# Performance work log

Measured on AMD Instinct MI355X. Metric: run time of the kernel, lower is better.

The kernel has to match this reference:

```python
import jax, jax.numpy as jnp
import numpy as np
from jax import lax

# Constants matching PostProcess(conf_thres=0.4, iou_thres=0.5, merge=False, agnostic=False)
CONF_THRES = 0.4
IOU_THRES = 0.5
MAX_WH = 4096.0   # per-class box offset (agnostic=False)
MAX_DET = 300     # hardcoded in module
MAX_NMS = 30000   # cap on NMS candidates (yolov5 convention); JAX needs static shapes
B, N, NC = 16, 25200, 80


def setup_inputs() -> dict:
    key = jax.random.key(0)
    u = jax.random.uniform(key, (B, N, 5 + NC), dtype=jnp.float32)
    # cx,cy in [0,640); w,h in [2,102); obj and class scores in [0,1)
    scale = jnp.concatenate([jnp.array([640.0, 640.0, 100.0, 100.0], jnp.float32),
                             jnp.ones((1 + NC,), jnp.float32)])
    shift = jnp.concatenate([jnp.array([0.0, 0.0, 2.0, 2.0], jnp.float32),
                             jnp.zeros((1 + NC,), jnp.float32)])
    prediction = u * scale + shift
    return {"prediction": prediction}


def _cxcywh_to_xyxy(x):
    cx, cy, w, h = x[..., 0], x[..., 1], x[..., 2], x[..., 3]
    return jnp.stack([cx - 0.5 * w, cy - 0.5 * h, cx + 0.5 * w, cy + 0.5 * h], axis=-1)


def _process_one(x):  # x: [N, 5+NC]
    obj = x[:, 4]
    cls_conf = x[:, 5:] * obj[:, None]          # x[:,5:] *= x[:,4:5]
    box = _cxcywh_to_xyxy(x[:, :4])             # [N, 4]
    # multi-label candidate mask: obj > conf AND class conf > conf (x[xc] then x[:,5:] > conf)
    cand = (obj[:, None] > CONF_THRES) & (cls_conf > CONF_THRES)   # [N, NC]
    flat = jnp.where(cand, cls_conf, 0.0).reshape(-1)              # [N*NC]
    top_scores, top_idx = lax.top_k(flat, MAX_NMS)                 # static-size candidate set
    bi = top_idx // NC                                             # box index i
    cj = (top_idx % NC).astype(jnp.float32)                        # class index j
    cand_boxes = box[bi]                                           # [M, 4]
    scores0 = jnp.where(top_scores > CONF_THRES, top_scores, 0.0)  # 0 marks invalid/suppressed
    off_boxes = cand_boxes + cj[:, None] * MAX_WH                  # per-class offset for NMS
    areas = (off_boxes[:, 2] - off_boxes[:, 0]) * (off_boxes[:, 3] - off_boxes[:, 1])
    idx_range = jnp.arange(MAX_NMS)

    def step(scores, _):
        # greedy NMS: pick best remaining, suppress IoU > thresh (torchvision semantics)
        idx = jnp.argmax(scores)
        s = scores[idx]
        keep = s > 0.0
        b = off_boxes[idx]
        lt = jnp.maximum(b[:2], off_boxes[:, :2])
        rb = jnp.minimum(b[2:], off_boxes[:, 2:])
        wh = jnp.clip(rb - lt, 0.0)
        inter = wh[:, 0] * wh[:, 1]
        iou = inter / (areas[idx] + areas - inter + 1e-9)
        suppress = (iou > IOU_THRES) | (idx_range == idx)
        return jnp.where(suppress, 0.0, scores), (idx, keep)

    _, (keep_idx, keep_flag) = lax.scan(step, scores0, None, length=MAX_DET)
    rows = jnp.concatenate([cand_boxes[keep_idx],
                            top_scores[keep_idx][:, None],
                            cj[keep_idx][:, None]], axis=1)        # [MAX_DET, 6] = xyxy, conf, cls
    return jnp.where(keep_flag[:, None], rows, 0.0)


def reference(prediction):
    # Padded fixed-shape analogue of torch.stack(output): [B, MAX_DET, 6], zero rows = no detection
    return jax.vmap(_process_one)(prediction)
```

## Files before the change

kernel.cpp:

```cpp
#include <hip/hip_runtime.h>
#include <stdint.h>

#define BATCH 16
#define NROW 25200
#define NCLS 80
#define ROWF 85
#define MAXDET 300
#define MAXNMS 30000u
#define NBIN 3072
#define BASEBITS 0x3EC00000u
#define CAP 32768u
#define BATCH_FLOATS 2142000

#define PREBIN 2048
#define NBUCK 1024
#define CANDCAP 131072u
#define KMAX 2048u
#define TOPK 2048u
#define K2CAP 4096u

#define SORTCAP 1024
#define CH_SZ 128

#define TILE_ROWS 80
#define TILE_FLOATS 6800
#define RPB 400
#define SUBT 5
#define SBLK 63

#define ROWS_PER_BLK 256
#define SBLK2 99

__device__ __forceinline__ bool iou_gt_half(float ax1, float ay1, float ax2, float ay2, float aa,
                                            float bx1, float by1, float bx2, float by2, float ba) {
    float ltx = fmaxf(ax1, bx1), lty = fmaxf(ay1, by1);
    float rbx = fminf(ax2, bx2), rby = fminf(ay2, by2);
    float wx = fmaxf(__fsub_rn(rbx, ltx), 0.0f);
    float wy = fmaxf(__fsub_rn(rby, lty), 0.0f);
    float inter = __fmul_rn(wx, wy);
    float den = __fadd_rn(__fsub_rn(__fadd_rn(aa, ba), inter), 1e-9f);
    float t = __fmul_rn(0.5f, den);
    if (!(inter > t)) return false;
    float tg = __fmul_rn(0.50000012f, den);
    if (inter >= tg) return true;
    return __fdiv_rn(inter, den) > 0.5f;
}

__device__ __forceinline__ unsigned bin_of_bits(unsigned bits) {
    unsigned v = (bits - BASEBITS) >> 12;
    if (v > (unsigned)(NBIN - 1)) v = NBIN - 1;
    return v;
}

__global__ __launch_bounds__(256) void k_stage(const float* __restrict__ pred,
                                               unsigned* __restrict__ hist2,
                                               unsigned* __restrict__ ccnt,
                                               unsigned long long* __restrict__ cand,
                                               unsigned* __restrict__ oflow,
                                               int staged) {
    if (!staged) return;
    __shared__ unsigned shist[NBUCK];
    __shared__ unsigned long long skey[KMAX];
    __shared__ unsigned s_cnt, s_n, s_base;
    int bx = blockIdx.x;
    int b = bx / SBLK2, blk = bx - b * SBLK2;
    int t = threadIdx.x, lane = t & 63, wv = t >> 6;
    for (int i = t; i < NBUCK; i += 256) shist[i] = 0u;
    if (t == 0) s_cnt = 0u;
    __syncthreads();
    const float* pb = pred + (size_t)b * BATCH_FLOATS;
    int r0 = blk * ROWS_PER_BLK + wv * 64;
    int rown = NROW - r0;
    if (rown > 0) {
        if (rown > 64) rown = 64;
        float obj = 0.0f;
        if (lane < rown) obj = pb[(size_t)(r0 + lane) * ROWF + 4];
        unsigned long long live = __ballot(obj > 0.4f);
        while (live) {
            int j = (int)__builtin_ctzll(live);
            live &= live - 1ULL;
            float o = __shfl(obj, j);
            const float* rp = pb + (size_t)(r0 + j) * ROWF;
            unsigned grow = (unsigned)(r0 + j);
            {
                float s = __fmul_rn(rp[5 + lane], o);
                if (s >= 0.75f) {
                    unsigned bits = __float_as_uint(s);
                    unsigned bin = bin_of_bits(bits);
                    atomicAdd(&shist[bin - PREBIN], 1u);
                    unsigned u = atomicAdd(&s_cnt, 1u);
                    unsigned flat = grow * (unsigned)NCLS + (unsigned)lane;
                    if (u < KMAX)
                        skey[u] = ((unsigned long long)bits << 32) |
                                  (unsigned long long)(0xFFFFFFFFu - flat);
                    else oflow[b] = 1u;
                }
            }
            if (lane < 16) {
                int c = 64 + lane;
                float s = __fmul_rn(rp[5 + c], o);
                if (s >= 0.75f) {
                    unsigned bits = __float_as_uint(s);
                    unsigned bin = bin_of_bits(bits);
                    atomicAdd(&shist[bin - PREBIN], 1u);
                    unsigned u = atomicAdd(&s_cnt, 1u);
                    unsigned flat = grow * (unsigned)NCLS + (unsigned)c;
                    if (u < KMAX)
                        skey[u] = ((unsigned long long)bits << 32) |
                                  (unsigned long long)(0xFFFFFFFFu - flat);
                    else oflow[b] = 1u;
                }
            }
        }
    }
    __syncthreads();
    unsigned* gh = hist2 + (size_t)b * NBUCK;
    for (int i = t; i < NBUCK; i += 256) {
        unsigned v = shist[i];
        if (v) atomicAdd(&gh[i], v);
    }
    if (t == 0) {
        unsigned n = s_cnt;
        if (n > KMAX) n = KMAX;
        unsigned base = atomicAdd(&ccnt[b], n);
        if (base + n > CANDCAP) oflow[b] = 1u;
        s_n = n; s_base = base;
    }
    __syncthreads();
    unsigned n = s_n, base = s_base;
    if (base + n <= CANDCAP) {
        unsigned long long* cd = cand + (size_t)b * CANDCAP + base;
        for (unsigned k = t; k < n; k += 256) cd[k] = skey[k];
    }
}

__global__ __launch_bounds__(1024) void k_prep(const unsigned* __restrict__ hist2,
                                               const unsigned* __restrict__ ccnt,
                                               const unsigned* __restrict__ oflow,
                                               const unsigned long long* __restrict__ cand,
                                               unsigned* __restrict__ suf2,
                                               unsigned long long* __restrict__ keys2,
                                               int* __restrict__ meta,
                                               int staged) {
    __shared__ unsigned sS[NBUCK];
    __shared__ unsigned scur[NBUCK];
    __shared__ int s_cut, s_need, s_tot, s_T, s_valid;
    __shared__ unsigned s_bad, s_E;
    int b = blockIdx.x, t = threadIdx.x;
    unsigned h = hist2[(size_t)b * NBUCK + t];
    sS[t] = h;
    if (t == 0) { s_cut = -1; s_T = -1; s_bad = 0u; s_need = 0; s_tot = 0; s_E = 0u; }
    __syncthreads();
    if (h > (unsigned)SORTCAP) atomicOr(&s_bad, 1u);
    for (int off = 1; off < NBUCK; off <<= 1) {
        unsigned v = (t + off < NBUCK) ? sS[t + off] : 0u;
        __syncthreads();
        sS[t] += v;
        __syncthreads();
    }
    unsigned Sv = sS[t];
    unsigned Sn = (t + 1 < NBUCK) ? sS[t + 1] : 0u;
    if (Sv >= MAXNMS && Sn < MAXNMS) {
        s_cut = PREBIN + t; s_need = (int)(MAXNMS - Sn); s_tot = (int)Sv;
    }
    if (Sv >= TOPK && Sn < TOPK) { s_T = PREBIN + t; s_E = Sv; }
    unsigned* g2 = suf2 + (size_t)b * (NBUCK + 1);
    g2[t] = Sv;
    if (t == 0) g2[NBUCK] = 0u;
    scur[t] = Sn;
    __syncthreads();
    if (t == 0) {
        int valid = (staged && s_cut >= 0 && s_T >= 0 && s_bad == 0u &&
                     oflow[b] == 0u && ccnt[b] <= CANDCAP) ? 1 : 0;
        s_valid = valid;
        meta[b * 8 + 0] = valid ? s_cut : 0;
        meta[b * 8 + 1] = valid ? s_need : 0;
        meta[b * 8 + 2] = valid ? s_tot : 0;
        meta[b * 8 + 3] = valid;
        meta[b * 8 + 4] = valid ? s_T : 0;
        meta[b * 8 + 5] = valid ? (int)s_E : 0;
    }
    __syncthreads();
    if (s_valid) {
        int T = s_T;
        unsigned ccb = ccnt[b];
        const unsigned long long* cd = cand + (size_t)b * CANDCAP;
        unsigned long long* k2 = keys2 + (size_t)b * K2CAP;
        for (unsigned k = t; k < ccb; k += 1024) {
            unsigned long long key = cd[k];
            unsigned v = bin_of_bits((unsigned)(key >> 32));
            if ((int)v >= T) {
                unsigned pos = atomicAdd(&scur[v - PREBIN], 1u);
                if (pos < K2CAP) k2[pos] = key;
            }
        }
    }
}

__global__ __launch_bounds__(256) void k_hist_fb(const float* __restrict__ pred,
                                                 unsigned* __restrict__ hist,
                                                 const int* __restrict__ meta) {
    int bx = blockIdx.x;
    int b = bx / SBLK, blk = bx - b * SBLK;
    if (meta[b * 8 + 3]) return;
    __shared__ __align__(16) float rows[TILE_FLOATS];
    __shared__ unsigned shist[NBIN];
    int t = threadIdx.x, lane = t & 63, wv = t >> 6;
    for (int i = t; i < NBIN; i += 256) shist[i] = 0u;
    const float* pbase = pred + (size_t)b * BATCH_FLOATS + (size_t)blk * RPB * ROWF;
    for (int st = 0; st < SUBT; ++st) {
        __syncthreads();
        const float4* src = (const float4*)(pbase + (size_t)st * TILE_ROWS * ROWF);
        float4* dst = (float4*)rows;
        for (int i = t; i < TILE_FLOATS / 4; i += 256) dst[i] = src[i];
        __syncthreads();
        for (int r = wv; r < TILE_ROWS; r += 4) {
            float obj = rows[r * ROWF + 4];
            if (!(obj > 0.4f)) continue;
            for (int half = 0; half < 2; ++half) {
                int c = lane + (half << 6);
                if (c < NCLS) {
                    float s = __fmul_rn(rows[r * ROWF + 5 + c], obj);
                    if (s > 0.4f) atomicAdd(&shist[bin_of_bits(__float_as_uint(s))], 1u);
                }
            }
        }
    }
    __syncthreads();
    unsigned* gh = hist + (size_t)b * NBIN;
    for (int i = t; i < NBIN; i += 256) {
        unsigned v = shist[i];
        if (v) atomicAdd(&gh[i], v);
    }
}

__global__ __launch_bounds__(256) void k_scan_fb(const unsigned* __restrict__ hist,
                                                 unsigned* __restrict__ suf,
                                                 int* __restrict__ meta) {
    int b = blockIdx.x, t = threadIdx.x;
    if (meta[b * 8 + 3]) return;
    __shared__ unsigned sh[NBIN];
    __shared__ unsigned sS[NBIN];
    __shared__ unsigned cs[256];
    __shared__ int s_cut, s_need, s_tot;
    const unsigned* gh = hist + (size_t)b * NBIN;
    for (int i = t; i < NBIN; i += 256) sh[i] = gh[i];
    if (t == 0) { s_cut = 0; s_need = 0x7FFFFFFF; s_tot = 0; }
    __syncthreads();
    const int CHUNK = NBIN / 256;
    int base = t * CHUNK;
    unsigned tot = 0;
    for (int i = 0; i < CHUNK; ++i) tot += sh[base + i];
    cs[t] = tot;
    __syncthreads();
    for (int off = 1; off < 256; off <<= 1) {
        unsigned v = (t + off < 256) ? cs[t + off] : 0u;
        __syncthreads();
        cs[t] += v;
        __syncthreads();
    }
    unsigned after = (t + 1 < 256) ? cs[t + 1] : 0u;
    for (int i = CHUNK - 1; i >= 0; --i) {
        after += sh[base + i];
        sS[base + i] = after;
    }
    __syncthreads();
    unsigned* gs = suf + (size_t)b * (NBIN + 1);
    for (int i = t; i < NBIN; i += 256) gs[i] = sS[i];
    if (t == 0) gs[NBIN] = 0u;
    for (int i = 0; i < CHUNK; ++i) {
        int v = base + i;
        unsigned Sv = sS[v];
        unsigned Sn = (v + 1 < NBIN) ? sS[v + 1] : 0u;
        if (Sv >= MAXNMS && Sn < MAXNMS) {
            s_cut = v; s_need = (int)(MAXNMS - Sn); s_tot = (int)Sv;
        }
    }
    __syncthreads();
    if (t == 0) {
        int cut = s_cut, needv = s_need, totv = s_tot;
        if (sS[0] < MAXNMS) { cut = 0; needv = 0x7FFFFFFF; totv = (int)sS[0]; }
        meta[b * 8 + 0] = cut;
        meta[b * 8 + 1] = needv;
        meta[b * 8 + 2] = totv;
    }
}

__global__ __launch_bounds__(256) void k_scatter_fb(const float* __restrict__ pred,
                                                    const unsigned* __restrict__ suf,
                                                    const int* __restrict__ meta,
                                                    unsigned* __restrict__ cursor,
                                                    unsigned long long* __restrict__ keys) {
    int bx = blockIdx.x;
    int b = bx / SBLK, blk = bx - b * SBLK;
    if (meta[b * 8 + 3]) return;
    __shared__ __align__(16) float rows[TILE_FLOATS];
    int t = threadIdx.x, lane = t & 63, wv = t >> 6;
    int cutbin = meta[b * 8 + 0];
    const float* pbase = pred + (size_t)b * BATCH_FLOATS + (size_t)blk * RPB * ROWF;
    unsigned rowbase0 = (unsigned)(blk * RPB);
    const unsigned* gs = suf + (size_t)b * (NBIN + 1);
    unsigned* cur = cursor + (size_t)b * NBIN;
    unsigned long long* kb = keys + (size_t)b * CAP;
    for (int st = 0; st < SUBT; ++st) {
        __syncthreads();
        const float4* src = (const float4*)(pbase + (size_t)st * TILE_ROWS * ROWF);
        float4* dst = (float4*)rows;
        for (int i = t; i < TILE_FLOATS / 4; i += 256) dst[i] = src[i];
        __syncthreads();
        for (int r = wv; r < TILE_ROWS; r += 4) {
            float obj = rows[r * ROWF + 4];
            if (!(obj > 0.4f)) continue;
            unsigned grow = rowbase0 + (unsigned)(st * TILE_ROWS + r);
            for (int half = 0; half < 2; ++half) {
                int c = lane + (half << 6);
                if (c < NCLS) {
                    float s = __fmul_rn(rows[r * ROWF + 5 + c], obj);
                    if (s > 0.4f) {
                        unsigned bits = __float_as_uint(s);
                        unsigned bin = bin_of_bits(bits);
                        if ((int)bin >= cutbin) {
                            unsigned pos = gs[bin + 1] + atomicAdd(&cur[bin], 1u);
                            if (pos < CAP) {
                                unsigned flat = grow * (unsigned)NCLS + (unsigned)c;
                                kb[pos] = ((unsigned long long)bits << 32) |
                                          (unsigned long long)(0xFFFFFFFFu - flat);
                            }
                        }
                    }
                }
            }
        }
    }
}

__global__ __launch_bounds__(1024) void k_nms(const float* __restrict__ pred,
                                              const unsigned* __restrict__ suf,
                                              const unsigned* __restrict__ suf2,
                                              const int* __restrict__ meta,
                                              const unsigned* __restrict__ ccnt,
                                              const unsigned long long* __restrict__ keys,
                                              const unsigned long long* __restrict__ keys2,
                                              const unsigned long long* __restrict__ cand,
                                              float* __restrict__ out) {
    __shared__ unsigned sgsL[NBUCK + 1];
    __shared__ unsigned long long ktmp[SORTCAP];
    __shared__ unsigned long long skeys[SORTCAP];
    __shared__ unsigned maskW[CH_SZ][5];
    __shared__ unsigned sup0w[4];
    __shared__ float cbox[CH_SZ][9];
    __shared__ float kept[MAXDET][5];
    __shared__ int klist[MAXDET];
    __shared__ int s_nk, s_localk;
    __shared__ unsigned s_gc;

    int b = blockIdx.x;
    int tid = threadIdx.x;
    int lane = tid & 63, wv = tid >> 6;

    int cutbin = meta[b * 8 + 0];
    int needv  = meta[b * 8 + 1];
    unsigned total = (unsigned)meta[b * 8 + 2];
    int valid  = meta[b * 8 + 3];
    int Tbin   = meta[b * 8 + 4];
    unsigned E = valid ? (unsigned)meta[b * 8 + 5] : 0u;
    if (!valid && total > CAP) total = CAP;
    const unsigned* gs = suf + (size_t)b * (NBIN + 1);
    const unsigned* g2 = suf2 + (size_t)b * (NBUCK + 1);
    const unsigned long long* kb = keys + (size_t)b * CAP;
    const unsigned long long* k2 = keys2 + (size_t)b * K2CAP;
    const unsigned long long* cd = cand + (size_t)b * CANDCAP;
    unsigned ccb = valid ? ccnt[b] : 0u;
    if (ccb > CANDCAP) ccb = CANDCAP;
    const float* pb = pred + (size_t)b * BATCH_FLOATS;
    float* ob = out + (size_t)b * MAXDET * 6;

    if (valid) for (int i = tid; i < NBUCK + 1; i += 1024) sgsL[i] = g2[i];
    if (tid == 0) s_nk = 0;
    __syncthreads();

#define GSV(v) (valid ? sgsL[(v) - PREBIN] : gs[(v)])

    unsigned limit;
    if (needv == 0x7FFFFFFF) limit = total;
    else limit = GSV(cutbin + 1) + (unsigned)needv;
    if (limit > total) limit = total;

    unsigned p = 0;
    while (p < limit) {
        if (s_nk >= MAXDET) break;

        int lo = cutbin, hi = NBIN - 1, vs = NBIN - 1;
        while (lo <= hi) { int mid = (lo + hi) >> 1;
            if (GSV(mid) <= p + (unsigned)SORTCAP) { vs = mid; hi = mid - 1; } else lo = mid + 1; }
        unsigned gEnd = GSV(vs);
        bool phaseA = (!valid) || (p < E);
        if (valid && phaseA && gEnd > E) gEnd = E;
        if (gEnd > total) gEnd = total;
        if (gEnd <= p) { gEnd = p + (unsigned)SORTCAP; if (gEnd > total) gEnd = total; }
        unsigned G = gEnd - p;

        if (phaseA) {
            const unsigned long long* src = valid ? k2 : kb;
            unsigned myLo = 0, myHi = 0;
            unsigned long long raw = 0ULL;
            if (tid < (int)G) {
                unsigned idx = p + (unsigned)tid;
                int l2 = cutbin, h2 = NBIN - 1, v = cutbin;
                while (l2 <= h2) { int mid = (l2 + h2) >> 1;
                    if (GSV(mid) > idx) { v = mid; l2 = mid + 1; } else h2 = mid - 1; }
                unsigned bstart = GSV(v + 1);
                unsigned bend = GSV(v);
                raw = src[idx];
                myLo = (bstart > p) ? (bstart - p) : 0u;
                myHi = bend - p; if (myHi > G) myHi = G;
                ktmp[tid] = raw;
            }
            __syncthreads();
            if (tid < (int)G) {
                unsigned rank = 0;
                for (unsigned u = myLo; u < myHi; ++u) rank += (ktmp[u] > raw) ? 1u : 0u;
                skeys[myLo + rank] = raw;
            }
            __syncthreads();
        } else {
            int l0 = cutbin, h0 = NBIN - 1, w1 = cutbin;
            while (l0 <= h0) { int mid = (l0 + h0) >> 1;
                if (GSV(mid) > p) { w1 = mid; l0 = mid + 1; } else h0 = mid - 1; }
            if (tid == 0) s_gc = 0u;
            __syncthreads();
            for (unsigned k = tid; k < ccb; k += 1024) {
                unsigned long long key = cd[k];
                unsigned v = bin_of_bits((unsigned)(key >> 32));
                if ((int)v >= vs && (int)v <= w1) {
                    unsigned u = atomicAdd(&s_gc, 1u);
                    if (u < (unsigned)SORTCAP) ktmp[u] = key;
                }
            }
            __syncthreads();
            unsigned Gc = s_gc; if (Gc > (unsigned)SORTCAP) Gc = (unsigned)SORTCAP;
            if (tid < (int)Gc) {
                unsigned long long key = ktmp[tid];
                unsigned v = bin_of_bits((unsigned)(key >> 32));
                unsigned bstart = GSV(v + 1);
                unsigned rank = 0;
                for (unsigned u = 0; u < Gc; ++u) {
                    unsigned long long kk = ktmp[u];
                    unsigned vu = bin_of_bits((unsigned)(kk >> 32));
                    rank += (vu == v && kk > key) ? 1u : 0u;
                }
                skeys[(bstart - p) + rank] = key;
            }
            __syncthreads();
        }

        unsigned consumable = limit - p; if (consumable > G) consumable = G;

        for (unsigned c0 = 0; c0 < consumable; c0 += CH_SZ) {
            int nk0 = s_nk;
            if (nk0 >= MAXDET) break;
            int CH = (int)((consumable - c0 < (unsigned)CH_SZ) ? (consumable - c0) : (unsigned)CH_SZ);

            if (tid < CH_SZ * 5) maskW[tid / 5][tid % 5] = 0u;
            if (tid >= CH_SZ * 5 && tid < CH_SZ * 5 + 4) sup0w[tid - CH_SZ * 5] = 0u;
            if (tid < CH) {
                unsigned long long kk = skeys[c0 + tid];
                unsigned flat = 0xFFFFFFFFu - (unsigned)kk;
                unsigned bi = flat / (unsigned)NCLS;
                unsigned cc = flat - bi * (unsigned)NCLS;
                const float* rp = pb + (size_t)bi * ROWF;
                float cx = rp[0], cy = rp[1], wd = rp[2], ht = rp[3];
                float hw = __fmul_rn(0.5f, wd), hh = __fmul_rn(0.5f, ht);
                float off = __fmul_rn((float)cc, 4096.0f);
                float x1 = __fsub_rn(cx, hw), y1 = __fsub_rn(cy, hh);
                float x2 = __fadd_rn(cx, hw), y2 = __fadd_rn(cy, hh);
                float ox1 = __fadd_rn(x1, off), oy1 = __fadd_rn(y1, off);
                float ox2 = __fadd_rn(x2, off), oy2 = __fadd_rn(y2, off);
                cbox[tid][0] = ox1; cbox[tid][1] = oy1;
                cbox[tid][2] = ox2; cbox[tid][3] = oy2;
                cbox[tid][4] = __fmul_rn(__fsub_rn(ox2, ox1), __fsub_rn(oy2, oy1));
            }
            __syncthreads();

            {
                int col = tid & (CH_SZ - 1);
                int part = tid >> 7;
                if (col < CH) {
                    float bx1 = cbox[col][0], by1 = cbox[col][1];
                    float bx2 = cbox[col][2], by2 = cbox[col][3], ba = cbox[col][4];
                    unsigned part16 = 0u;
                    int rbase = part << 4;
                    for (int k = 0; k < 16; ++k) {
                        int i2 = rbase + k;
                        if (i2 >= col || i2 >= CH) break;
                        if (iou_gt_half(cbox[i2][0], cbox[i2][1], cbox[i2][2], cbox[i2][3],
                                        cbox[i2][4], bx1, by1, bx2, by2, ba))
                            part16 |= (1u << k);
                    }
                    if (part16)
                        atomicOr(&maskW[col][part >> 1], part16 << ((part & 1) << 4));
                    bool f = false;
                    for (int k2 = part; k2 < nk0; k2 += 8) {
                        if (iou_gt_half(kept[k2][0], kept[k2][1], kept[k2][2], kept[k2][3],
                                        kept[k2][4], bx1, by1, bx2, by2, ba)) f = true;
                    }
                    if (f) atomicOr(&sup0w[col >> 5], 1u << (col & 31));
                }
            }
            __syncthreads();

            if (wv == 0) {
                unsigned keptw = 0u;
                int nkv = nk0, lk = 0;
                unsigned pre0 = (lane < 4 && CH > 0) ? maskW[0][lane] : 0u;
                unsigned pre1 = (lane < 4 && CH > 1) ? maskW[1][lane] : 0u;
                for (int j = 0; j < CH && nkv < MAXDET; ++j) {
                    unsigned colw = pre0;
                    pre0 = pre1;
                    pre1 = (lane < 4 && (j + 2) < CH) ? maskW[j + 2][lane] : 0u;
                    bool hit = (keptw & colw) != 0u;
                    bool sup = __any(hit);
                    if ((sup0w[j >> 5] >> (j & 31)) & 1u) sup = true;
                    if (!sup) {
                        if (lane == (j >> 5)) keptw |= 1u << (j & 31);
                        if (lane == 0) klist[lk] = j;
                        lk++; nkv++;
                    }
                }
                if (lane == 0) { s_localk = lk; s_nk = nkv; }
            }
            __syncthreads();

            int lk = s_localk;
            for (int t2 = tid; t2 < lk; t2 += 1024) {
                int i = klist[t2];
                int oidx = nk0 + t2;
                kept[oidx][0] = cbox[i][0]; kept[oidx][1] = cbox[i][1];
                kept[oidx][2] = cbox[i][2]; kept[oidx][3] = cbox[i][3];
                kept[oidx][4] = cbox[i][4];
                unsigned long long kk = skeys[c0 + i];
                unsigned bits = (unsigned)(kk >> 32);
                unsigned flat = 0xFFFFFFFFu - (unsigned)kk;
                unsigned bi = flat / (unsigned)NCLS;
                unsigned cc = flat - bi * (unsigned)NCLS;
                const float* rp = pb + (size_t)bi * ROWF;
                float cx = rp[0], cy = rp[1], wd = rp[2], ht = rp[3];
                float hw = __fmul_rn(0.5f, wd), hh = __fmul_rn(0.5f, ht);
                float* orow = ob + (size_t)oidx * 6;
                orow[0] = __fsub_rn(cx, hw);
                orow[1] = __fsub_rn(cy, hh);
                orow[2] = __fadd_rn(cx, hw);
                orow[3] = __fadd_rn(cy, hh);
                orow[4] = __uint_as_float(bits);
                orow[5] = (float)cc;
            }
            __syncthreads();
        }
        p = gEnd;
    }
#undef GSV
}

extern "C" void kernel_launch(void* const* d_in, const int* in_sizes, int n_in,
                              void* d_out, int out_size, void* d_ws, size_t ws_size,
                              hipStream_t stream) {
    const float* pred = (const float*)d_in[0];
    float* outp = (float*)d_out;
    char* ws = (char*)d_ws;

    const size_t OFF_HIST  = 0;
    const size_t SZ_HIST   = (size_t)BATCH * NBIN * 4;
    const size_t OFF_CUR   = OFF_HIST + SZ_HIST;
    const size_t SZ_CUR    = (size_t)BATCH * NBIN * 4;
    const size_t OFF_H2    = OFF_CUR + SZ_CUR;
    const size_t SZ_H2     = (size_t)BATCH * NBUCK * 4;
    const size_t OFF_CCNT  = OFF_H2 + SZ_H2;
    const size_t SZ_CCNT   = (size_t)BATCH * 4;
    const size_t OFF_OFLW  = OFF_CCNT + SZ_CCNT;
    const size_t SZ_OFLW   = (size_t)BATCH * 4;
    const size_t OFF_META  = OFF_OFLW + SZ_OFLW;
    const size_t SZ_META   = (size_t)BATCH * 8 * 4;
    const size_t ZERO_SZ   = OFF_META + SZ_META;
    const size_t OFF_SUF   = ZERO_SZ;
    const size_t SZ_SUF    = (size_t)BATCH * (NBIN + 1) * 4;
    const size_t OFF_SUF2  = OFF_SUF + SZ_SUF;
    const size_t SZ_SUF2   = (size_t)BATCH * (NBUCK + 1) * 4;
    const size_t OFF_KEYS  = OFF_SUF2 + SZ_SUF2;
    const size_t SZ_KEYS   = (size_t)BATCH * CAP * 8;
    const size_t OFF_K2    = OFF_KEYS + SZ_KEYS;
    const size_t SZ_K2     = (size_t)BATCH * K2CAP * 8;
    const size_t OFF_CAND  = OFF_K2 + SZ_K2;
    const size_t SZ_CAND   = (size_t)BATCH * CANDCAP * 8;
    const size_t WS_NEEDED = OFF_CAND + SZ_CAND;

    int staged = (ws_size >= WS_NEEDED) ? 1 : 0;

    unsigned* hist             = (unsigned*)(ws + OFF_HIST);
    unsigned* cursor           = (unsigned*)(ws + OFF_CUR);
    unsigned* hist2            = (unsigned*)(ws + OFF_H2);
    unsigned* ccnt             = (unsigned*)(ws + OFF_CCNT);
    unsigned* oflow            = (unsigned*)(ws + OFF_OFLW);
    int* meta                  = (int*)(ws + OFF_META);
    unsigned* suf              = (unsigned*)(ws + OFF_SUF);
    unsigned* suf2             = (unsigned*)(ws + OFF_SUF2);
    unsigned long long* keys   = (unsigned long long*)(ws + OFF_KEYS);
    unsigned long long* keys2  = (unsigned long long*)(ws + OFF_K2);
    unsigned long long* cand   = (unsigned long long*)(ws + OFF_CAND);

    hipMemsetAsync(ws, 0, ZERO_SZ, stream);
    hipMemsetAsync(d_out, 0, (size_t)out_size * sizeof(float), stream);

    k_stage<<<dim3(BATCH * SBLK2), dim3(256), 0, stream>>>(pred, hist2, ccnt, cand, oflow, staged);
    k_prep<<<dim3(BATCH), dim3(1024), 0, stream>>>(hist2, ccnt, oflow, cand, suf2, keys2, meta, staged);
    k_hist_fb<<<dim3(BATCH * SBLK), dim3(256), 0, stream>>>(pred, hist, meta);
    k_scan_fb<<<dim3(BATCH), dim3(256), 0, stream>>>(hist, suf, meta);
    k_scatter_fb<<<dim3(BATCH * SBLK), dim3(256), 0, stream>>>(pred, suf, meta, cursor, keys);
    k_nms<<<dim3(BATCH), dim3(1024), 0, stream>>>(pred, suf, suf2, meta, ccnt, keys, keys2, cand, outp);
}
```

Baseline: 347.7 us.

## Flatten stage scan over elements and split candidate scatter into parallel kernel

The staging kernel now walks flat (row, class) elements across 128 blocks per batch, dropping the per-row obj ballot and early-skip, so every class element is read. The candidate scatter that used to run at the end of the single-block-per-batch prep kernel moves to a new kernel with 16 blocks per batch that uses global-memory atomics on bucket cursors. The aim is more parallelism in both phases. In exchange it loses the skip of rows with low objectness, reads the obj value once per element, adds global atomics and one more launch.

Result: no change. 349.8 us (+0.6%).

```diff
diff --git a/kernel.cpp b/kernel.cpp
--- a/kernel.cpp
+++ b/kernel.cpp
@@ -11,6 +11,7 @@
 #define BASEBITS 0x3EC00000u
 #define CAP 32768u
 #define BATCH_FLOATS 2142000
+#define NELEM 2016000u
 
 #define PREBIN 2048
 #define NBUCK 1024
@@ -22,14 +23,14 @@
 #define SORTCAP 1024
 #define CH_SZ 128
 
+#define SBLK3 128
+#define EPB (NELEM / SBLK3)
+
 #define TILE_ROWS 80
 #define TILE_FLOATS 6800
 #define RPB 400
 #define SUBT 5
 #define SBLK 63
-
-#define ROWS_PER_BLK 256
-#define SBLK2 99
 
 __device__ __forceinline__ bool iou_gt_half(float ax1, float ay1, float ax2, float ay2, float aa,
                                             float bx1, float by1, float bx2, float by2, float ba) {
@@ -63,54 +64,30 @@
     __shared__ unsigned long long skey[KMAX];
     __shared__ unsigned s_cnt, s_n, s_base;
     int bx = blockIdx.x;
-    int b = bx / SBLK2, blk = bx - b * SBLK2;
-    int t = threadIdx.x, lane = t & 63, wv = t >> 6;
+    int b = bx >> 7, blk = bx & (SBLK3 - 1);
+    int t = threadIdx.x;
     for (int i = t; i < NBUCK; i += 256) shist[i] = 0u;
     if (t == 0) s_cnt = 0u;
     __syncthreads();
     const float* pb = pred + (size_t)b * BATCH_FLOATS;
-    int r0 = blk * ROWS_PER_BLK + wv * 64;
-    int rown = NROW - r0;
-    if (rown > 0) {
-        if (rown > 64) rown = 64;
-        float obj = 0.0f;
-        if (lane < rown) obj = pb[(size_t)(r0 + lane) * ROWF + 4];
-        unsigned long long live = __ballot(obj > 0.4f);
-        while (live) {
-            int j = (int)__builtin_ctzll(live);
-            live &= live - 1ULL;
-            float o = __shfl(obj, j);
-            const float* rp = pb + (size_t)(r0 + j) * ROWF;
-            unsigned grow = (unsigned)(r0 + j);
-            {
-                float s = __fmul_rn(rp[5 + lane], o);
-                if (s >= 0.75f) {
-                    unsigned bits = __float_as_uint(s);
-                    unsigned bin = bin_of_bits(bits);
-                    atomicAdd(&shist[bin - PREBIN], 1u);
-                    unsigned u = atomicAdd(&s_cnt, 1u);
-                    unsigned flat = grow * (unsigned)NCLS + (unsigned)lane;
-                    if (u < KMAX)
-                        skey[u] = ((unsigned long long)bits << 32) |
-                                  (unsigned long long)(0xFFFFFFFFu - flat);
-                    else oflow[b] = 1u;
-                }
-            }
-            if (lane < 16) {
-                int c = 64 + lane;
-                float s = __fmul_rn(rp[5 + c], o);
-                if (s >= 0.75f) {
-                    unsigned bits = __float_as_uint(s);
-                    unsigned bin = bin_of_bits(bits);
-                    atomicAdd(&shist[bin - PREBIN], 1u);
-                    unsigned u = atomicAdd(&s_cnt, 1u);
-                    unsigned flat = grow * (unsigned)NCLS + (unsigned)c;
-                    if (u < KMAX)
-                        skey[u] = ((unsigned long long)bits << 32) |
-                                  (unsigned long long)(0xFFFFFFFFu - flat);
-                    else oflow[b] = 1u;
-                }
-            }
+    unsigned e0 = (unsigned)blk * EPB, e1 = e0 + EPB;
+    for (unsigned e = e0 + (unsigned)t; e < e1; e += 256u) {
+        unsigned row = e / (unsigned)NCLS;
+        unsigned c = e - row * (unsigned)NCLS;
+        unsigned rb = row * (unsigned)ROWF;
+        float obj = pb[rb + 4u];
+        float cv  = pb[rb + 5u + c];
+        float s = __fmul_rn(cv, obj);
+        if (s >= 0.75f) {
+            unsigned bits = __float_as_uint(s);
+            unsigned bin = bin_of_bits(bits);
+            atomicAdd(&shist[bin - PREBIN], 1u);
+            unsigned u = atomicAdd(&s_cnt, 1u);
+            unsigned flat = e;
+            if (u < KMAX)
+                skey[u] = ((unsigned long long)bits << 32) |
+                          (unsigned long long)(0xFFFFFFFFu - flat);
+            else oflow[b] = 1u;
         }
     }
     __syncthreads();
@@ -137,14 +114,12 @@
 __global__ __launch_bounds__(1024) void k_prep(const unsigned* __restrict__ hist2,
                                                const unsigned* __restrict__ ccnt,
                                                const unsigned* __restrict__ oflow,
-                                               const unsigned long long* __restrict__ cand,
                                                unsigned* __restrict__ suf2,
-                                               unsigned long long* __restrict__ keys2,
+                                               unsigned* __restrict__ gcur,
                                                int* __restrict__ meta,
                                                int staged) {
     __shared__ unsigned sS[NBUCK];
-    __shared__ unsigned scur[NBUCK];
-    __shared__ int s_cut, s_need, s_tot, s_T, s_valid;
+    __shared__ int s_cut, s_need, s_tot, s_T;
     __shared__ unsigned s_bad, s_E;
     int b = blockIdx.x, t = threadIdx.x;
     unsigned h = hist2[(size_t)b * NBUCK + t];
@@ -167,12 +142,11 @@
     unsigned* g2 = suf2 + (size_t)b * (NBUCK + 1);
     g2[t] = Sv;
     if (t == 0) g2[NBUCK] = 0u;
-    scur[t] = Sn;
+    gcur[(size_t)b * NBUCK + t] = Sn;
     __syncthreads();
     if (t == 0) {
         int valid = (staged && s_cut >= 0 && s_T >= 0 && s_bad == 0u &&
                      oflow[b] == 0u && ccnt[b] <= CANDCAP) ? 1 : 0;
-        s_valid = valid;
         meta[b * 8 + 0] = valid ? s_cut : 0;
         meta[b * 8 + 1] = valid ? s_need : 0;
         meta[b * 8 + 2] = valid ? s_tot : 0;
@@ -180,19 +154,31 @@
         meta[b * 8 + 4] = valid ? s_T : 0;
         meta[b * 8 + 5] = valid ? (int)s_E : 0;
     }
-    __syncthreads();
-    if (s_valid) {
-        int T = s_T;
-        unsigned ccb = ccnt[b];
-        const unsigned long long* cd = cand + (size_t)b * CANDCAP;
-        unsigned long long* k2 = keys2 + (size_t)b * K2CAP;
-        for (unsigned k = t; k < ccb; k += 1024) {
-            unsigned long long key = cd[k];
-            unsigned v = bin_of_bits((unsigned)(key >> 32));
-            if ((int)v >= T) {
-                unsigned pos = atomicAdd(&scur[v - PREBIN], 1u);
-                if (pos < K2CAP) k2[pos] = key;
-            }
+}
+
+__global__ __launch_bounds__(256) void k_scat2(const unsigned long long* __restrict__ cand,
+                                               const unsigned* __restrict__ ccnt,
+                                               const int* __restrict__ meta,
+                                               unsigned* __restrict__ gcur,
+                                               unsigned long long* __restrict__ keys2) {
+    int bx = blockIdx.x;
+    int b = bx >> 4, blk = bx & 15;
+    if (!meta[b * 8 + 3]) return;
+    int T = meta[b * 8 + 4];
+    unsigned ccb = ccnt[b];
+    if (ccb > CANDCAP) ccb = CANDCAP;
+    unsigned per = (ccb + 15u) >> 4;
+    unsigned s0 = (unsigned)blk * per, s1 = s0 + per;
+    if (s1 > ccb) s1 = ccb;
+    const unsigned long long* cd = cand + (size_t)b * CANDCAP;
+    unsigned long long* k2 = keys2 + (size_t)b * K2CAP;
+    unsigned* gc = gcur + (size_t)b * NBUCK;
+    for (unsigned k = s0 + threadIdx.x; k < s1; k += 256) {
+        unsigned long long key = cd[k];
+        unsigned v = bin_of_bits((unsigned)(key >> 32));
+        if ((int)v >= T) {
+            unsigned pos = atomicAdd(&gc[v - PREBIN], 1u);
+            if (pos < K2CAP) k2[pos] = key;
         }
     }
 }
@@ -362,7 +348,6 @@
     int needv  = meta[b * 8 + 1];
     unsigned total = (unsigned)meta[b * 8 + 2];
     int valid  = meta[b * 8 + 3];
-    int Tbin   = meta[b * 8 + 4];
     unsigned E = valid ? (unsigned)meta[b * 8 + 5] : 0u;
     if (!valid && total > CAP) total = CAP;
     const unsigned* gs = suf + (size_t)b * (NBIN + 1);
@@ -500,9 +485,9 @@
                     if (part16)
                         atomicOr(&maskW[col][part >> 1], part16 << ((part & 1) << 4));
                     bool f = false;
-                    for (int k2 = part; k2 < nk0; k2 += 8) {
-                        if (iou_gt_half(kept[k2][0], kept[k2][1], kept[k2][2], kept[k2][3],
-                                        kept[k2][4], bx1, by1, bx2, by2, ba)) f = true;
+                    for (int k2i = part; k2i < nk0; k2i += 8) {
+                        if (iou_gt_half(kept[k2i][0], kept[k2i][1], kept[k2i][2], kept[k2i][3],
+                                        kept[k2i][4], bx1, by1, bx2, by2, ba)) f = true;
                     }
                     if (f) atomicOr(&sup0w[col >> 5], 1u << (col & 31));
                 }
@@ -585,7 +570,9 @@
     const size_t SZ_SUF    = (size_t)BATCH * (NBIN + 1) * 4;
     const size_t OFF_SUF2  = OFF_SUF + SZ_SUF;
     const size_t SZ_SUF2   = (size_t)BATCH * (NBUCK + 1) * 4;
-    const size_t OFF_KEYS  = OFF_SUF2 + SZ_SUF2;
+    const size_t OFF_GCUR  = OFF_SUF2 + SZ_SUF2;
+    const size_t SZ_GCUR   = (size_t)BATCH * NBUCK * 4;
+    const size_t OFF_KEYS  = OFF_GCUR + SZ_GCUR;
     const size_t SZ_KEYS   = (size_t)BATCH * CAP * 8;
     const size_t OFF_K2    = OFF_KEYS + SZ_KEYS;
     const size_t SZ_K2     = (size_t)BATCH * K2CAP * 8;
@@ -603,6 +590,7 @@
     int* meta                  = (int*)(ws + OFF_META);
     unsigned* suf              = (unsigned*)(ws + OFF_SUF);
     unsigned* suf2             = (unsigned*)(ws + OFF_SUF2);
+    unsigned* gcur             = (unsigned*)(ws + OFF_GCUR);
     unsigned long long* keys   = (unsigned long long*)(ws + OFF_KEYS);
     unsigned long long* keys2  = (unsigned long long*)(ws + OFF_K2);
     unsigned long long* cand   = (unsigned long long*)(ws + OFF_CAND);
@@ -610,8 +598,9 @@
     hipMemsetAsync(ws, 0, ZERO_SZ, stream);
     hipMemsetAsync(d_out, 0, (size_t)out_size * sizeof(float), stream);
 
-    k_stage<<<dim3(BATCH * SBLK2), dim3(256), 0, stream>>>(pred, hist2, ccnt, cand, oflow, staged);
-    k_prep<<<dim3(BATCH), dim3(1024), 0, stream>>>(hist2, ccnt, oflow, cand, suf2, keys2, meta, staged);
+    k_stage<<<dim3(BATCH * SBLK3), dim3(256), 0, stream>>>(pred, hist2, ccnt, cand, oflow, staged);
+    k_prep<<<dim3(BATCH), dim3(1024), 0, stream>>>(hist2, ccnt, oflow, suf2, gcur, meta, staged);
+    k_scat2<<<dim3(BATCH * 16), dim3(256), 0, stream>>>(cand, ccnt, meta, gcur, keys2);
     k_hist_fb<<<dim3(BATCH * SBLK), dim3(256), 0, stream>>>(pred, hist, meta);
     k_scan_fb<<<dim3(BATCH), dim3(256), 0, stream>>>(hist, suf, meta);
     k_scatter_fb<<<dim3(BATCH * SBLK), dim3(256), 0, stream>>>(pred, suf, meta, cursor, keys);
```
